# Kernel tuning notes

Measured on AMD Instinct MI355X. Metric: run time of the kernel, lower is better.

The kernel has to match this reference:

```python
import jax, jax.numpy as jnp
import numpy as np

N, E, D, H, DH, FF, C, L = 50000, 640000, 128, 8, 16, 256, 5, 6
EPS = 1e-5


def _bn(x, g, b):
    # training-mode BatchNorm1d over the node dimension
    m = jnp.mean(x, axis=0)
    v = jnp.var(x, axis=0)
    return (x - m) * jax.lax.rsqrt(v + EPS) * g + b


def _sparse_mha(x, src, dst, Wq, Wk, Wv, Wo):
    # edge-restricted multi-head attention: softmax over incoming edges per dst node
    q = (x @ Wq).reshape(N, H, DH)
    k = (x @ Wk).reshape(N, H, DH)
    v = (x @ Wv).reshape(N, H, DH)
    s = jnp.einsum('ehd,ehd->eh', q[dst], k[src]) * (1.0 / np.sqrt(DH))  # [E,H]
    smax = jax.ops.segment_max(s, dst, num_segments=N)
    smax = jnp.where(jnp.isfinite(smax), smax, 0.0)  # guard isolated nodes
    e = jnp.exp(s - smax[dst])
    den = jax.ops.segment_sum(e, dst, num_segments=N)
    alpha = e / jnp.where(den > 0, den, 1.0)[dst]
    out = jax.ops.segment_sum(alpha[:, :, None] * v[src], dst, num_segments=N)  # [N,H,DH]
    return out.reshape(N, D) @ Wo


def setup_inputs() -> dict:
    key = jax.random.key(0)
    ks = jax.random.split(key, 18)
    f = lambda k, shp, sc: (jax.random.normal(k, shp, jnp.float32) * sc)
    return {
        'x': jax.random.normal(ks[0], (N, D), jnp.float32),
        'edge_index': jax.random.randint(ks[1], (2, E), 0, N),
        'Wq': f(ks[2], (L, D, D), 0.08),
        'Wk': f(ks[3], (L, D, D), 0.08),
        'Wv': f(ks[4], (L, D, D), 0.08),
        'Wo': f(ks[5], (L, D, D), 0.08),
        'g1': jnp.ones((L, D), jnp.float32),
        'bn1': jnp.zeros((L, D), jnp.float32),
        'W1': f(ks[6], (L, D, FF), 0.08),
        'bf1': jnp.zeros((L, FF), jnp.float32),
        'W2': f(ks[7], (L, FF, D), 0.06),
        'bf2': jnp.zeros((L, D), jnp.float32),
        'g2': jnp.ones((L, D), jnp.float32),
        'bn2': jnp.zeros((L, D), jnp.float32),
        'Wp': f(ks[8], (D, C), 0.08),
        'bp': jnp.zeros((C,), jnp.float32),
    }


def reference(x, edge_index, Wq, Wk, Wv, Wo, g1, bn1, W1, bf1, W2, bf2, g2, bn2, Wp, bp):
    src, dst = edge_index[0], edge_index[1]
    for i in range(L):  # fixed small layer count
        res = x  # residual is Identity (num_input == num_output)
        a = _sparse_mha(x, src, dst, Wq[i], Wk[i], Wv[i], Wo[i])
        x = _bn(a + res, g1[i], bn1[i])
        h = jax.nn.relu(x @ W1[i] + bf1[i])  # leakiness=0 -> relu
        x = _bn(x + (h @ W2[i] + bf2[i]), g2[i], bn2[i])
    node_pred = x @ Wp + bp
    return node_pred
```

## Files before the change

kernel.cpp:

```cpp
#include <hip/hip_runtime.h>
#include <hip/hip_bf16.h>
#include <cstdio>

#define NN 50000
#define EE 640000
#define DD 128
#define HH 8
#define DH 16
#define FFD 256
#define CC 5
#define LL 6
#define EPSV 1e-5f

typedef __attribute__((ext_vector_type(8))) short bf16x8;
typedef __attribute__((ext_vector_type(8))) unsigned short ushort8;
typedef __attribute__((ext_vector_type(4))) float f32x4;

__device__ __forceinline__ float bfu2f(unsigned short u) {
  union { unsigned int i; float f; } x; x.i = ((unsigned int)u) << 16; return x.f;
}
__device__ __forceinline__ unsigned short f2bf(float f) {
  union { float f; unsigned int i; } x; x.f = f;
  unsigned int r = (x.i + 0x7fffu + ((x.i >> 16) & 1u)) >> 16;
  return (unsigned short)r;
}

__global__ void detect_kernel(const unsigned int* __restrict__ g1w, int* __restrict__ flag) {
  if (threadIdx.x == 0 && blockIdx.x == 0) *flag = (g1w[0] == 0x3F803F80u) ? 1 : 0;
}

struct ConvJobs { const void* in[8]; float* out[8]; int n[8]; };
__global__ __launch_bounds__(256) void convert_batch_kernel(ConvJobs jobs, const int* __restrict__ flag) {
  int b = blockIdx.x;
  const void* in = jobs.in[b];
  float* out = jobs.out[b];
  int n = jobs.n[b];
  int use_bf = *flag;
  for (int i = threadIdx.x; i < n; i += 256) {
    if (use_bf) out[i] = bfu2f(((const unsigned short*)in)[i]);
    else        out[i] = ((const float*)in)[i];
  }
}

__global__ __launch_bounds__(256) void to_bf16_kernel(const void* __restrict__ in,
                                                      unsigned short* __restrict__ out, int n,
                                                      const int* __restrict__ flag) {
  int i = blockIdx.x * blockDim.x + threadIdx.x;
  if (i >= n) return;
  if (*flag) out[i] = ((const unsigned short*)in)[i];
  else       out[i] = f2bf(((const float*)in)[i]);
}

__global__ __launch_bounds__(256) void t_qkv_tiled(const void* __restrict__ wq, const void* __restrict__ wk,
                                                   const void* __restrict__ wv,
                                                   unsigned short* __restrict__ qkvT,
                                                   const int* __restrict__ flag) {
  __shared__ unsigned short tile[32][33];
  int l = blockIdx.z / 3, which = blockIdx.z % 3;
  const void* in = (which == 0) ? wq : (which == 1) ? wk : wv;
  size_t off = (size_t)l * DD * DD;
  unsigned short* out = qkvT + (size_t)l * 384 * DD + (size_t)which * DD * DD;
  int tx = threadIdx.x & 31, ty = threadIdx.x >> 5;
  int k0 = blockIdx.x * 32, n0 = blockIdx.y * 32;
  int use_bf = *flag;
#pragma unroll
  for (int i = 0; i < 4; i++) {
    int k = k0 + ty + i * 8;
    unsigned short v;
    if (use_bf) v = ((const unsigned short*)in)[off + (size_t)k * DD + n0 + tx];
    else        v = f2bf(((const float*)in)[off + (size_t)k * DD + n0 + tx]);
    tile[ty + i * 8][tx] = v;
  }
  __syncthreads();
#pragma unroll
  for (int i = 0; i < 4; i++) {
    int n = n0 + ty + i * 8;
    out[(size_t)n * DD + k0 + tx] = tile[tx][ty + i * 8];
  }
}

__global__ __launch_bounds__(256) void t_w_tiled(const void* __restrict__ in,
                                                 unsigned short* __restrict__ out,
                                                 int K, int N, const int* __restrict__ flag) {
  __shared__ unsigned short tile[32][33];
  int l = blockIdx.z;
  size_t off = (size_t)l * K * N;
  unsigned short* o = out + (size_t)l * K * N;
  int tx = threadIdx.x & 31, ty = threadIdx.x >> 5;
  int k0 = blockIdx.x * 32, n0 = blockIdx.y * 32;
  int use_bf = *flag;
#pragma unroll
  for (int i = 0; i < 4; i++) {
    int k = k0 + ty + i * 8;
    unsigned short v;
    if (use_bf) v = ((const unsigned short*)in)[off + (size_t)k * N + n0 + tx];
    else        v = f2bf(((const float*)in)[off + (size_t)k * N + n0 + tx]);
    tile[ty + i * 8][tx] = v;
  }
  __syncthreads();
#pragma unroll
  for (int i = 0; i < 4; i++) {
    int n = n0 + ty + i * 8;
    o[(size_t)n * K + k0 + tx] = tile[tx][ty + i * 8];
  }
}

__global__ __launch_bounds__(256) void zero_kernel(int* __restrict__ p, int n) {
  int i = blockIdx.x * blockDim.x + threadIdx.x;
  if (i < n) p[i] = 0;
}

__global__ void init_id_kernel(float* __restrict__ stats_id, float* __restrict__ g_id, float* __restrict__ b_id) {
  int t = threadIdx.x;
  if (t < 128) {
    stats_id[t] = 0.f;
    stats_id[128 + t] = (float)NN * (1.0f - EPSV);
    g_id[t] = 1.f;
    b_id[t] = 0.f;
  }
}

__global__ __launch_bounds__(256) void count_kernel(const int* __restrict__ dst, int* __restrict__ counts) {
  int e = blockIdx.x * blockDim.x + threadIdx.x;
  if (e < EE) atomicAdd(&counts[dst[e]], 1);
}

__global__ __launch_bounds__(256) void scan1_kernel(const int* __restrict__ counts,
                                                    int* __restrict__ row_ptr, int* __restrict__ partials) {
  __shared__ int sh[256];
  int t = threadIdx.x;
  int i = blockIdx.x * 256 + t;
  int v = (i < NN) ? counts[i] : 0;
  sh[t] = v; __syncthreads();
#pragma unroll
  for (int off = 1; off < 256; off <<= 1) {
    int u = (t >= off) ? sh[t - off] : 0;
    __syncthreads();
    sh[t] += u;
    __syncthreads();
  }
  if (i < NN) row_ptr[i] = sh[t] - v;
  if (t == 255) partials[blockIdx.x] = sh[t];
}

__global__ __launch_bounds__(256) void scan2_kernel(int* __restrict__ partials, int nb) {
  __shared__ int sh[256];
  int t = threadIdx.x;
  int v = (t < nb) ? partials[t] : 0;
  sh[t] = v; __syncthreads();
#pragma unroll
  for (int off = 1; off < 256; off <<= 1) {
    int u = (t >= off) ? sh[t - off] : 0;
    __syncthreads();
    sh[t] += u;
    __syncthreads();
  }
  if (t < nb) partials[t] = sh[t] - v;
}

__global__ __launch_bounds__(256) void scan3_kernel(int* __restrict__ row_ptr, const int* __restrict__ partials) {
  int i = blockIdx.x * 256 + threadIdx.x;
  if (i < NN) row_ptr[i] += partials[blockIdx.x];
  if (i == 0) row_ptr[NN] = EE;
}

__global__ __launch_bounds__(256) void fill_kernel(const int* __restrict__ src, const int* __restrict__ dst,
                                                   const int* __restrict__ row_ptr, int* __restrict__ cursor,
                                                   int* __restrict__ csr_src) {
  int e = blockIdx.x * blockDim.x + threadIdx.x;
  if (e < EE) {
    int d = dst[e];
    int pos = row_ptr[d] + atomicAdd(&cursor[d], 1);
    csr_src[pos] = src[e];
  }
}

__global__ __launch_bounds__(128) void fold_kernel(const float* __restrict__ stats,
                                                   const float* __restrict__ g,
                                                   const float* __restrict__ b,
                                                   const unsigned short* __restrict__ WT,
                                                   const float* __restrict__ base_bias,
                                                   unsigned short* __restrict__ WTo,
                                                   float* __restrict__ bias_o,
                                                   float* __restrict__ ss_o) {
  __shared__ float ssc[128];
  __shared__ float ssh[128];
  __shared__ float part[2];
  int t = threadIdx.x;
  float mean = stats[t] * (1.f / NN);
  float var  = fmaxf(stats[128 + t] * (1.f / NN) - mean * mean, 0.f);
  float sc = g[t] * rsqrtf(var + EPSV);
  float sh = b[t] - mean * sc;
  ssc[t] = sc; ssh[t] = sh;
  if (blockIdx.x == 0) { ss_o[t] = sc; ss_o[128 + t] = sh; }
  __syncthreads();
  int c = blockIdx.x;
  float w = bfu2f(WT[(size_t)c * 128 + t]);
  WTo[(size_t)c * 128 + t] = f2bf(ssc[t] * w);
  float contrib = ssh[t] * w;
#pragma unroll
  for (int off = 32; off; off >>= 1) contrib += __shfl_down(contrib, off);
  if ((t & 63) == 0) part[t >> 6] = contrib;
  __syncthreads();
  if (t == 0) bias_o[c] = (base_bias ? base_bias[c] : 0.f) + part[0] + part[1];
}

template<int NTILES, bool RELU>
__global__ __launch_bounds__(256) void mfma_gemm_nt(const unsigned short* __restrict__ A,
                                                    const unsigned short* __restrict__ BT,
                                                    const float* __restrict__ bias,
                                                    unsigned short* __restrict__ C,
                                                    int M, int ldc) {
  const int K = 128;
  int tid = threadIdx.x;
  int lane = tid & 63, wave = tid >> 6;
  int m0 = blockIdx.x * 128 + wave * 32;
  int nbase = blockIdx.y * (NTILES * 64);
  int lm = lane & 15;
  int quad = lane >> 4;
  int kq = quad * 8;

  int rowA[2];
#pragma unroll
  for (int r = 0; r < 2; r++) {
    int rr = m0 + 16 * r + lm;
    rowA[r] = (rr < M) ? rr : (M - 1);
  }
  bf16x8 a[2][4];
#pragma unroll
  for (int ks = 0; ks < 4; ks++) {
    a[0][ks] = *(const bf16x8*)(A + (size_t)rowA[0] * K + ks * 32 + kq);
    a[1][ks] = *(const bf16x8*)(A + (size_t)rowA[1] * K + ks * 32 + kq);
  }

#pragma unroll
  for (int nt = 0; nt < NTILES; nt++) {
    int n0 = nbase + nt * 64;
    bf16x8 b[4][4];
#pragma unroll
    for (int c = 0; c < 4; c++)
#pragma unroll
      for (int ks = 0; ks < 4; ks++)
        b[c][ks] = *(const bf16x8*)(BT + (size_t)(n0 + 16 * c + lm) * K + ks * 32 + kq);

    f32x4 acc[2][4];
#pragma unroll
    for (int r = 0; r < 2; r++)
#pragma unroll
      for (int c = 0; c < 4; c++) acc[r][c] = (f32x4){0.f, 0.f, 0.f, 0.f};
#pragma unroll
    for (int ks = 0; ks < 4; ks++)
#pragma unroll
      for (int r = 0; r < 2; r++)
#pragma unroll
        for (int c = 0; c < 4; c++)
          acc[r][c] = __builtin_amdgcn_mfma_f32_16x16x32_bf16(b[c][ks], a[r][ks], acc[r][c], 0, 0, 0);

#pragma unroll
    for (int r = 0; r < 2; r++) {
      int row = m0 + 16 * r + lm;
      if (row >= M) continue;
#pragma unroll
      for (int c = 0; c < 4; c++) {
        int col = n0 + 16 * c + quad * 4;
        float4 bv = *(const float4*)(bias + col);
        float o[4];
        o[0] = acc[r][c][0] + bv.x; o[1] = acc[r][c][1] + bv.y;
        o[2] = acc[r][c][2] + bv.z; o[3] = acc[r][c][3] + bv.w;
        if (RELU) {
          o[0] = fmaxf(o[0], 0.f); o[1] = fmaxf(o[1], 0.f);
          o[2] = fmaxf(o[2], 0.f); o[3] = fmaxf(o[3], 0.f);
        }
        ushort4 w;
        w.x = f2bf(o[0]); w.y = f2bf(o[1]); w.z = f2bf(o[2]); w.w = f2bf(o[3]);
        *(ushort4*)(C + (size_t)row * ldc + col) = w;
      }
    }
  }
}

template<int K, bool RELU, bool HASBIAS, bool RESAFF, bool STATS>
__global__ __launch_bounds__(256) void mfma_gemm(const unsigned short* __restrict__ A,
                                                 const unsigned short* __restrict__ BT,
                                                 const float* __restrict__ bias,
                                                 const unsigned short* __restrict__ resid,
                                                 const float* __restrict__ rss,
                                                 unsigned short* __restrict__ C,
                                                 float* __restrict__ stats,
                                                 int M, int ldc) {
  __shared__ float lsum[64];
  __shared__ float lsq[64];
  int tid = threadIdx.x;
  int lane = tid & 63, wave = tid >> 6;
  int m0 = blockIdx.x * 128 + wave * 32;
  int n0 = blockIdx.y * 64;
  int lm = lane & 15;
  int quad = lane >> 4;
  int kq = quad * 8;

  int rowA[2];
#pragma unroll
  for (int r = 0; r < 2; r++) {
    int rr = m0 + 16 * r + lm;
    rowA[r] = (rr < M) ? rr : (M - 1);
  }
  const unsigned short* aptr0 = A + (size_t)rowA[0] * K + kq;
  const unsigned short* aptr1 = A + (size_t)rowA[1] * K + kq;
  const unsigned short* bptr[4];
#pragma unroll
  for (int c = 0; c < 4; c++)
    bptr[c] = BT + (size_t)(n0 + 16 * c + lm) * K + kq;

  f32x4 acc[2][4];
#pragma unroll
  for (int r = 0; r < 2; r++)
#pragma unroll
    for (int c = 0; c < 4; c++) acc[r][c] = (f32x4){0.f, 0.f, 0.f, 0.f};

#pragma unroll
  for (int kc = 0; kc < K; kc += 128) {
    bf16x8 a[2][4], b[4][4];
#pragma unroll
    for (int ks = 0; ks < 4; ks++) {
      a[0][ks] = *(const bf16x8*)(aptr0 + kc + ks * 32);
      a[1][ks] = *(const bf16x8*)(aptr1 + kc + ks * 32);
    }
#pragma unroll
    for (int c = 0; c < 4; c++)
#pragma unroll
      for (int ks = 0; ks < 4; ks++)
        b[c][ks] = *(const bf16x8*)(bptr[c] + kc + ks * 32);
#pragma unroll
    for (int ks = 0; ks < 4; ks++)
#pragma unroll
      for (int r = 0; r < 2; r++)
#pragma unroll
        for (int c = 0; c < 4; c++)
          acc[r][c] = __builtin_amdgcn_mfma_f32_16x16x32_bf16(b[c][ks], a[r][ks], acc[r][c], 0, 0, 0);
  }

  if (STATS) {
    if (tid < 64) { lsum[tid] = 0.f; lsq[tid] = 0.f; }
    __syncthreads();
  }

  float st_s[4][4], st_q[4][4];
  if (STATS) {
#pragma unroll
    for (int c = 0; c < 4; c++)
#pragma unroll
      for (int reg = 0; reg < 4; reg++) { st_s[c][reg] = 0.f; st_q[c][reg] = 0.f; }
  }

#pragma unroll
  for (int r = 0; r < 2; r++) {
    int row = m0 + 16 * r + lm;
    if (row >= M) continue;
#pragma unroll
    for (int c = 0; c < 4; c++) {
      int col = n0 + 16 * c + quad * 4;
      float4 bv = HASBIAS ? *(const float4*)(bias + col) : make_float4(0.f, 0.f, 0.f, 0.f);
      float o[4];
      o[0] = acc[r][c][0] + bv.x; o[1] = acc[r][c][1] + bv.y;
      o[2] = acc[r][c][2] + bv.z; o[3] = acc[r][c][3] + bv.w;
      if (RESAFF) {
        ushort4 rr = *(const ushort4*)(resid + (size_t)row * ldc + col);
        float4 rsc = *(const float4*)(rss + col);
        float4 rsh = *(const float4*)(rss + 128 + col);
        o[0] += bfu2f(rr.x) * rsc.x + rsh.x;
        o[1] += bfu2f(rr.y) * rsc.y + rsh.y;
        o[2] += bfu2f(rr.z) * rsc.z + rsh.z;
        o[3] += bfu2f(rr.w) * rsc.w + rsh.w;
      }
      if (RELU) {
        o[0] = fmaxf(o[0], 0.f); o[1] = fmaxf(o[1], 0.f);
        o[2] = fmaxf(o[2], 0.f); o[3] = fmaxf(o[3], 0.f);
      }
      size_t idx = (size_t)row * ldc + col;
      ushort4 w;
      w.x = f2bf(o[0]); w.y = f2bf(o[1]); w.z = f2bf(o[2]); w.w = f2bf(o[3]);
      *(ushort4*)(C + idx) = w;
      if (STATS) {
#pragma unroll
        for (int reg = 0; reg < 4; reg++) {
          st_s[c][reg] += o[reg];
          st_q[c][reg] = fmaf(o[reg], o[reg], st_q[c][reg]);
        }
      }
    }
  }

  if (STATS) {
#pragma unroll
    for (int c = 0; c < 4; c++)
#pragma unroll
      for (int reg = 0; reg < 4; reg++) {
        float s = st_s[c][reg], q = st_q[c][reg];
        s += __shfl_xor(s, 1);  q += __shfl_xor(q, 1);
        s += __shfl_xor(s, 2);  q += __shfl_xor(q, 2);
        s += __shfl_xor(s, 4);  q += __shfl_xor(q, 4);
        s += __shfl_xor(s, 8);  q += __shfl_xor(q, 8);
        if (lm == 0) {
          atomicAdd(&lsum[16 * c + quad * 4 + reg], s);
          atomicAdd(&lsq[16 * c + quad * 4 + reg], q);
        }
      }
    __syncthreads();
    if (tid < 64) {
      atomicAdd(&stats[n0 + tid], lsum[tid]);
      atomicAdd(&stats[128 + n0 + tid], lsq[tid]);
    }
  }
}

__global__ __launch_bounds__(256) void attn_kernel(const unsigned short* __restrict__ qkv,
                                                   const int* __restrict__ row_ptr,
                                                   const int* __restrict__ csr_src,
                                                   unsigned short* __restrict__ t1) {
  int t = blockIdx.x * blockDim.x + threadIdx.x;
  int half = t & 1;
  int nh = t >> 1;
  int n = nh >> 3, h = nh & 7;
  const unsigned short* qp = qkv + (size_t)n * 384 + h * 16 + half * 8;
  float qf[8];
  {
    bf16x8 q0 = *(const bf16x8*)qp;
#pragma unroll
    for (int i = 0; i < 8; i++) qf[i] = bfu2f((unsigned short)q0[i]);
  }
  float m = -3.0e38f, l = 0.f;
  float A[8];
#pragma unroll
  for (int i = 0; i < 8; i++) A[i] = 0.f;
  int e0 = row_ptr[n], e1 = row_ptr[n + 1];
  if (e0 < e1) {
    int last = e1 - 1;
    const size_t hoff = 128 + h * 16 + half * 8;
    int s0 = csr_src[e0];
    const unsigned short* kp0 = qkv + (size_t)s0 * 384 + hoff;
    bf16x8 ck = *(const bf16x8*)kp0;
    bf16x8 cv = *(const bf16x8*)(kp0 + 128);
    int ei1 = (e0 + 1 <= last) ? e0 + 1 : last;
    int s1 = csr_src[ei1];
    const unsigned short* kp1 = qkv + (size_t)s1 * 384 + hoff;
    bf16x8 nk = *(const bf16x8*)kp1;
    bf16x8 nv = *(const bf16x8*)(kp1 + 128);
    for (int e = e0; e < e1; e++) {
      int e2 = (e + 2 <= last) ? e + 2 : last;
      int s2 = csr_src[e2];
      const unsigned short* kp2 = qkv + (size_t)s2 * 384 + hoff;
      bf16x8 k2 = *(const bf16x8*)kp2;
      bf16x8 v2 = *(const bf16x8*)(kp2 + 128);

      float part = 0.f;
#pragma unroll
      for (int i = 0; i < 8; i++) part += qf[i] * bfu2f((unsigned short)ck[i]);
      float sc = (part + __shfl_xor(part, 1)) * 0.25f;
      float mn = fmaxf(m, sc);
      float cf = __expf(m - mn);
      float p  = __expf(sc - mn);
      l = l * cf + p;
#pragma unroll
      for (int i = 0; i < 8; i++)
        A[i] = A[i] * cf + p * bfu2f((unsigned short)cv[i]);
      m = mn;
      ck = nk; cv = nv; nk = k2; nv = v2;
    }
  }
  float inv = (l > 0.f) ? 1.f / l : 0.f;
  ushort8 o0;
#pragma unroll
  for (int i = 0; i < 8; i++) o0[i] = f2bf(A[i] * inv);
  unsigned short* op = t1 + (size_t)n * 128 + h * 16 + half * 8;
  *(ushort8*)op = o0;
}

__global__ __launch_bounds__(256) void proj_kernel(const unsigned short* __restrict__ y2,
                                                   const float* __restrict__ statsL,
                                                   const float* __restrict__ g,
                                                   const float* __restrict__ b,
                                                   const float* __restrict__ Wp,
                                                   const float* __restrict__ bp,
                                                   void* __restrict__ out,
                                                   const int* __restrict__ flag) {
  __shared__ float W[DD * CC];
  __shared__ float bias[CC];
  __shared__ float ssc[128];
  __shared__ float ssh[128];
  int t = threadIdx.x;
  for (int i = t; i < DD * CC; i += 256) W[i] = Wp[i];
  if (t < CC) bias[t] = bp[t];
  if (t < 128) {
    float mean = statsL[t] * (1.f / NN);
    float var  = fmaxf(statsL[128 + t] * (1.f / NN) - mean * mean, 0.f);
    float sc = g[t] * rsqrtf(var + EPSV);
    ssc[t] = sc;
    ssh[t] = b[t] - mean * sc;
  }
  __syncthreads();
  int n = blockIdx.x * 256 + t;
  if (n >= NN) return;
  float acc[CC];
#pragma unroll
  for (int c = 0; c < CC; c++) acc[c] = bias[c];
  const ushort4* xp = (const ushort4*)(y2 + (size_t)n * DD);
#pragma unroll
  for (int k4 = 0; k4 < DD / 4; k4++) {
    ushort4 u = xp[k4];
    int k = k4 * 4;
    float a0 = bfu2f(u.x) * ssc[k + 0] + ssh[k + 0];
    float a1 = bfu2f(u.y) * ssc[k + 1] + ssh[k + 1];
    float a2 = bfu2f(u.z) * ssc[k + 2] + ssh[k + 2];
    float a3 = bfu2f(u.w) * ssc[k + 3] + ssh[k + 3];
    const float* w = &W[k * CC];
#pragma unroll
    for (int c = 0; c < CC; c++)
      acc[c] += a0 * w[c] + a1 * w[CC + c] + a2 * w[2 * CC + c] + a3 * w[3 * CC + c];
  }
  if (*flag) {
    __hip_bfloat16* o16 = (__hip_bfloat16*)out;
#pragma unroll
    for (int c = 0; c < CC; c++) o16[(size_t)n * CC + c] = __float2bfloat16(acc[c]);
  } else {
    float* o32 = (float*)out;
#pragma unroll
    for (int c = 0; c < CC; c++) o32[(size_t)n * CC + c] = acc[c];
  }
}

extern "C" void kernel_launch(void* const* d_in, const int* in_sizes, int n_in,
                              void* d_out, int out_size, void* d_ws, size_t ws_size,
                              hipStream_t stream) {
  const int* ei = (const int*)d_in[1];

  char* p = (char*)d_ws;
  auto carve = [&](size_t bytes) { char* r = p; p += (bytes + 255) & ~(size_t)255; return (void*)r; };
  unsigned short* xb   = (unsigned short*)carve((size_t)NN * DD * 2);
  unsigned short* qkv  = (unsigned short*)carve((size_t)NN * 384 * 2);
  unsigned short* t1   = (unsigned short*)carve((size_t)NN * DD * 2);
  unsigned short* hbuf = (unsigned short*)carve((size_t)NN * FFD * 2);
  unsigned short* y1   = (unsigned short*)carve((size_t)NN * DD * 2);
  unsigned short* y2   = (unsigned short*)carve((size_t)NN * DD * 2);
  float* stats  = (float*)carve(12 * 256 * 4);
  float* stats_id = (float*)carve(256 * 4);
  float* ss     = (float*)carve(12 * 256 * 4);
  float* ss_id  = (float*)carve(256 * 4);
  float* g_id   = (float*)carve(128 * 4);
  float* b_id   = (float*)carve(128 * 4);
  int* row_ptr = (int*)carve((size_t)(NN + 1) * 4);
  int* cursor  = (int*)carve((size_t)NN * 4);
  int* counts  = (int*)carve((size_t)NN * 4);
  int* csr_src = (int*)carve((size_t)EE * 4);
  int* flag    = (int*)carve(256);
  int* partials = (int*)carve(256 * 4);
  unsigned short* qkvT = (unsigned short*)carve((size_t)LL * 384 * DD * 2);
  unsigned short* WoT  = (unsigned short*)carve((size_t)LL * DD * DD * 2);
  unsigned short* W1T  = (unsigned short*)carve((size_t)LL * FFD * DD * 2);
  unsigned short* W2T  = (unsigned short*)carve((size_t)LL * DD * FFD * 2);
  unsigned short* qkvTf = (unsigned short*)carve((size_t)384 * DD * 2);
  unsigned short* W1Tf  = (unsigned short*)carve((size_t)FFD * DD * 2);
  float* qkv_bias = (float*)carve(384 * 4);
  float* w1_bias  = (float*)carve(256 * 4);
  float* g1_f  = (float*)carve((size_t)LL * DD * 4);
  float* bn1_f = (float*)carve((size_t)LL * DD * 4);
  float* bf1_f = (float*)carve((size_t)LL * FFD * 4);
  float* bf2_f = (float*)carve((size_t)LL * DD * 4);
  float* g2_f  = (float*)carve((size_t)LL * DD * 4);
  float* bn2_f = (float*)carve((size_t)LL * DD * 4);
  float* Wp_f  = (float*)carve((size_t)DD * CC * 4);
  float* bp_f  = (float*)carve((size_t)CC * 4);
  size_t need = (size_t)(p - (char*)d_ws);
  if (need > ws_size) {
    fprintf(stderr, "kernel_launch: workspace too small: need %zu, have %zu\n", need, ws_size);
    return;
  }

  const int* src  = ei;
  const int* dstp = ei + EE;

  detect_kernel<<<1, 64, 0, stream>>>((const unsigned int*)d_in[6], flag);
  to_bf16_kernel<<<(NN * DD + 255) / 256, 256, 0, stream>>>(d_in[0], xb, NN * DD, flag);

  {
    ConvJobs j;
    j.in[0] = d_in[6];  j.out[0] = g1_f;  j.n[0] = LL * DD;
    j.in[1] = d_in[7];  j.out[1] = bn1_f; j.n[1] = LL * DD;
    j.in[2] = d_in[9];  j.out[2] = bf1_f; j.n[2] = LL * FFD;
    j.in[3] = d_in[11]; j.out[3] = bf2_f; j.n[3] = LL * DD;
    j.in[4] = d_in[12]; j.out[4] = g2_f;  j.n[4] = LL * DD;
    j.in[5] = d_in[13]; j.out[5] = bn2_f; j.n[5] = LL * DD;
    j.in[6] = d_in[14]; j.out[6] = Wp_f;  j.n[6] = DD * CC;
    j.in[7] = d_in[15]; j.out[7] = bp_f;  j.n[7] = CC;
    convert_batch_kernel<<<8, 256, 0, stream>>>(j, flag);
  }

  t_qkv_tiled<<<dim3(4, 4, 3 * LL), 256, 0, stream>>>(d_in[2], d_in[3], d_in[4], qkvT, flag);
  t_w_tiled<<<dim3(4, 4, LL), 256, 0, stream>>>(d_in[5], WoT, DD, DD, flag);
  t_w_tiled<<<dim3(4, 8, LL), 256, 0, stream>>>(d_in[8], W1T, DD, FFD, flag);
  t_w_tiled<<<dim3(8, 4, LL), 256, 0, stream>>>(d_in[10], W2T, FFD, DD, flag);

  zero_kernel<<<12, 256, 0, stream>>>((int*)stats, 12 * 256);
  init_id_kernel<<<1, 128, 0, stream>>>(stats_id, g_id, b_id);
  zero_kernel<<<(NN + 255) / 256, 256, 0, stream>>>(counts, NN);
  zero_kernel<<<(NN + 255) / 256, 256, 0, stream>>>(cursor, NN);

  const int NB = (NN + 255) / 256;
  count_kernel<<<(EE + 255) / 256, 256, 0, stream>>>(dstp, counts);
  scan1_kernel<<<NB, 256, 0, stream>>>(counts, row_ptr, partials);
  scan2_kernel<<<1, 256, 0, stream>>>(partials, NB);
  scan3_kernel<<<NB, 256, 0, stream>>>(row_ptr, partials);
  fill_kernel<<<(EE + 255) / 256, 256, 0, stream>>>(src, dstp, row_ptr, cursor, csr_src);

  const int gm = (NN + 127) / 128;
  for (int layer = 0; layer < LL; layer++) {
    const unsigned short* WoT_l = WoT + (size_t)layer * DD * DD;
    const unsigned short* W1T_l = W1T + (size_t)layer * FFD * DD;
    const unsigned short* W2T_l = W2T + (size_t)layer * DD * FFD;
    float* st1 = stats + (size_t)(layer * 2 + 0) * 256;
    float* st2 = stats + (size_t)(layer * 2 + 1) * 256;
    float* ss1 = ss + (size_t)(layer * 2 + 0) * 256;

    const unsigned short* Ain = layer ? y2 : xb;
    const float* stats_prev = layer ? (stats + (size_t)((layer - 1) * 2 + 1) * 256) : stats_id;
    const float* g_prev = layer ? (g2_f + (size_t)(layer - 1) * DD) : g_id;
    const float* b_prev = layer ? (bn2_f + (size_t)(layer - 1) * DD) : b_id;
    float* ss_prev = layer ? (ss + (size_t)((layer - 1) * 2 + 1) * 256) : ss_id;

    fold_kernel<<<384, 128, 0, stream>>>(stats_prev, g_prev, b_prev,
                                         qkvT + (size_t)layer * 384 * DD, nullptr,
                                         qkvTf, qkv_bias, ss_prev);
    mfma_gemm_nt<3, false><<<dim3(gm, 2), 256, 0, stream>>>(
        Ain, qkvTf, qkv_bias, qkv, NN, 384);
    attn_kernel<<<NN * HH * 2 / 256, 256, 0, stream>>>(qkv, row_ptr, csr_src, t1);
    mfma_gemm<128, false, false, true, true><<<dim3(gm, 2), 256, 0, stream>>>(
        t1, WoT_l, nullptr, Ain, ss_prev, y1, st1, NN, 128);
    fold_kernel<<<256, 128, 0, stream>>>(st1, g1_f + (size_t)layer * DD, bn1_f + (size_t)layer * DD,
                                         W1T_l, bf1_f + (size_t)layer * FFD,
                                         W1Tf, w1_bias, ss1);
    mfma_gemm_nt<2, true><<<dim3(gm, 2), 256, 0, stream>>>(
        y1, W1Tf, w1_bias, hbuf, NN, 256);
    mfma_gemm<256, false, true, true, true><<<dim3(gm, 2), 256, 0, stream>>>(
        hbuf, W2T_l, bf2_f + (size_t)layer * DD, y1, ss1, y2, st2, NN, 128);
  }

  proj_kernel<<<(NN + 255) / 256, 256, 0, stream>>>(
      y2, stats + (size_t)((LL - 1) * 2 + 1) * 256, g2_f + (size_t)(LL - 1) * DD,
      bn2_f + (size_t)(LL - 1) * DD, Wp_f, bp_f, d_out, flag);
}
```

Measured before the change: 1.389 ms.

## Fuse FFN GEMMs through LDS and route QKV projection through generic GEMM

Adds an ffn_fused kernel that computes relu(y1·W1+b1) into a padded LDS tile and immediately multiplies it by W2, adding the BN-affine residual and accumulating batch-norm statistics. The intermediate hidden activation no longer round-trips through global memory, and one launch per layer goes away. The QKV projection now uses the generic mfma_gemm with a 6-wide column grid instead of the removed NT kernel. The cost is about 67KB of LDS per block and a larger per-block workload, which reduces occupancy.

```diff
diff --git a/kernel.cpp b/kernel.cpp
--- a/kernel.cpp
+++ b/kernel.cpp
@@ -11,6 +11,7 @@
 #define CC 5
 #define LL 6
 #define EPSV 1e-5f
+#define HPAD 264
 
 typedef __attribute__((ext_vector_type(8))) short bf16x8;
 typedef __attribute__((ext_vector_type(8))) unsigned short ushort8;
@@ -203,80 +204,6 @@
   if ((t & 63) == 0) part[t >> 6] = contrib;
   __syncthreads();
   if (t == 0) bias_o[c] = (base_bias ? base_bias[c] : 0.f) + part[0] + part[1];
-}
-
-template<int NTILES, bool RELU>
-__global__ __launch_bounds__(256) void mfma_gemm_nt(const unsigned short* __restrict__ A,
-                                                    const unsigned short* __restrict__ BT,
-                                                    const float* __restrict__ bias,
-                                                    unsigned short* __restrict__ C,
-                                                    int M, int ldc) {
-  const int K = 128;
-  int tid = threadIdx.x;
-  int lane = tid & 63, wave = tid >> 6;
-  int m0 = blockIdx.x * 128 + wave * 32;
-  int nbase = blockIdx.y * (NTILES * 64);
-  int lm = lane & 15;
-  int quad = lane >> 4;
-  int kq = quad * 8;
-
-  int rowA[2];
-#pragma unroll
-  for (int r = 0; r < 2; r++) {
-    int rr = m0 + 16 * r + lm;
-    rowA[r] = (rr < M) ? rr : (M - 1);
-  }
-  bf16x8 a[2][4];
-#pragma unroll
-  for (int ks = 0; ks < 4; ks++) {
-    a[0][ks] = *(const bf16x8*)(A + (size_t)rowA[0] * K + ks * 32 + kq);
-    a[1][ks] = *(const bf16x8*)(A + (size_t)rowA[1] * K + ks * 32 + kq);
-  }
-
-#pragma unroll
-  for (int nt = 0; nt < NTILES; nt++) {
-    int n0 = nbase + nt * 64;
-    bf16x8 b[4][4];
-#pragma unroll
-    for (int c = 0; c < 4; c++)
-#pragma unroll
-      for (int ks = 0; ks < 4; ks++)
-        b[c][ks] = *(const bf16x8*)(BT + (size_t)(n0 + 16 * c + lm) * K + ks * 32 + kq);
-
-    f32x4 acc[2][4];
-#pragma unroll
-    for (int r = 0; r < 2; r++)
-#pragma unroll
-      for (int c = 0; c < 4; c++) acc[r][c] = (f32x4){0.f, 0.f, 0.f, 0.f};
-#pragma unroll
-    for (int ks = 0; ks < 4; ks++)
-#pragma unroll
-      for (int r = 0; r < 2; r++)
-#pragma unroll
-        for (int c = 0; c < 4; c++)
-          acc[r][c] = __builtin_amdgcn_mfma_f32_16x16x32_bf16(b[c][ks], a[r][ks], acc[r][c], 0, 0, 0);
-
-#pragma unroll
-    for (int r = 0; r < 2; r++) {
-      int row = m0 + 16 * r + lm;
-      if (row >= M) continue;
-#pragma unroll
-      for (int c = 0; c < 4; c++) {
-        int col = n0 + 16 * c + quad * 4;
-        float4 bv = *(const float4*)(bias + col);
-        float o[4];
-        o[0] = acc[r][c][0] + bv.x; o[1] = acc[r][c][1] + bv.y;
-        o[2] = acc[r][c][2] + bv.z; o[3] = acc[r][c][3] + bv.w;
-        if (RELU) {
-          o[0] = fmaxf(o[0], 0.f); o[1] = fmaxf(o[1], 0.f);
-          o[2] = fmaxf(o[2], 0.f); o[3] = fmaxf(o[3], 0.f);
-        }
-        ushort4 w;
-        w.x = f2bf(o[0]); w.y = f2bf(o[1]); w.z = f2bf(o[2]); w.w = f2bf(o[3]);
-        *(ushort4*)(C + (size_t)row * ldc + col) = w;
-      }
-    }
-  }
 }
 
 template<int K, bool RELU, bool HASBIAS, bool RESAFF, bool STATS>
@@ -413,6 +340,162 @@
   }
 }
 
+__global__ __launch_bounds__(256) void ffn_fused(const unsigned short* __restrict__ A,
+                                                 const unsigned short* __restrict__ W1T,
+                                                 const float* __restrict__ b1,
+                                                 const unsigned short* __restrict__ W2T,
+                                                 const float* __restrict__ b2,
+                                                 const float* __restrict__ rss,
+                                                 unsigned short* __restrict__ C,
+                                                 float* __restrict__ stats, int M) {
+  __shared__ unsigned short hl[128 * HPAD];
+  __shared__ float lsum[128];
+  __shared__ float lsq[128];
+  int tid = threadIdx.x;
+  int lane = tid & 63, wave = tid >> 6;
+  int m0 = blockIdx.x * 128 + wave * 32;
+  int lm = lane & 15, quad = lane >> 4, kq = quad * 8;
+
+  if (tid < 128) { lsum[tid] = 0.f; lsq[tid] = 0.f; }
+  __syncthreads();
+
+  int rowA[2];
+#pragma unroll
+  for (int r = 0; r < 2; r++) {
+    int rr = m0 + 16 * r + lm;
+    rowA[r] = (rr < M) ? rr : (M - 1);
+  }
+  bf16x8 a[2][4];
+#pragma unroll
+  for (int ks = 0; ks < 4; ks++) {
+    a[0][ks] = *(const bf16x8*)(A + (size_t)rowA[0] * 128 + ks * 32 + kq);
+    a[1][ks] = *(const bf16x8*)(A + (size_t)rowA[1] * 128 + ks * 32 + kq);
+  }
+
+#pragma unroll
+  for (int nt = 0; nt < 4; nt++) {
+    int n0 = nt * 64;
+    bf16x8 b[4][4];
+#pragma unroll
+    for (int c = 0; c < 4; c++)
+#pragma unroll
+      for (int ks = 0; ks < 4; ks++)
+        b[c][ks] = *(const bf16x8*)(W1T + (size_t)(n0 + 16 * c + lm) * 128 + ks * 32 + kq);
+    f32x4 acc[2][4];
+#pragma unroll
+    for (int r = 0; r < 2; r++)
+#pragma unroll
+      for (int c = 0; c < 4; c++) acc[r][c] = (f32x4){0.f, 0.f, 0.f, 0.f};
+#pragma unroll
+    for (int ks = 0; ks < 4; ks++)
+#pragma unroll
+      for (int r = 0; r < 2; r++)
+#pragma unroll
+        for (int c = 0; c < 4; c++)
+          acc[r][c] = __builtin_amdgcn_mfma_f32_16x16x32_bf16(b[c][ks], a[r][ks], acc[r][c], 0, 0, 0);
+#pragma unroll
+    for (int r = 0; r < 2; r++) {
+      int lrow = wave * 32 + 16 * r + lm;
+#pragma unroll
+      for (int c = 0; c < 4; c++) {
+        int col = n0 + 16 * c + quad * 4;
+        float4 bv = *(const float4*)(b1 + col);
+        ushort4 w;
+        w.x = f2bf(fmaxf(acc[r][c][0] + bv.x, 0.f));
+        w.y = f2bf(fmaxf(acc[r][c][1] + bv.y, 0.f));
+        w.z = f2bf(fmaxf(acc[r][c][2] + bv.z, 0.f));
+        w.w = f2bf(fmaxf(acc[r][c][3] + bv.w, 0.f));
+        *(ushort4*)(hl + (size_t)lrow * HPAD + col) = w;
+      }
+    }
+  }
+
+#pragma unroll
+  for (int nt = 0; nt < 2; nt++) {
+    int n0 = nt * 64;
+    f32x4 acc[2][4];
+#pragma unroll
+    for (int r = 0; r < 2; r++)
+#pragma unroll
+      for (int c = 0; c < 4; c++) acc[r][c] = (f32x4){0.f, 0.f, 0.f, 0.f};
+#pragma unroll
+    for (int kc = 0; kc < 256; kc += 128) {
+      bf16x8 ha[2][4], b[4][4];
+#pragma unroll
+      for (int ks = 0; ks < 4; ks++) {
+        ha[0][ks] = *(const bf16x8*)(hl + (size_t)(wave * 32 + lm) * HPAD + kc + ks * 32 + kq);
+        ha[1][ks] = *(const bf16x8*)(hl + (size_t)(wave * 32 + 16 + lm) * HPAD + kc + ks * 32 + kq);
+      }
+#pragma unroll
+      for (int c = 0; c < 4; c++)
+#pragma unroll
+        for (int ks = 0; ks < 4; ks++)
+          b[c][ks] = *(const bf16x8*)(W2T + (size_t)(n0 + 16 * c + lm) * 256 + kc + ks * 32 + kq);
+#pragma unroll
+      for (int ks = 0; ks < 4; ks++)
+#pragma unroll
+        for (int r = 0; r < 2; r++)
+#pragma unroll
+          for (int c = 0; c < 4; c++)
+            acc[r][c] = __builtin_amdgcn_mfma_f32_16x16x32_bf16(b[c][ks], ha[r][ks], acc[r][c], 0, 0, 0);
+    }
+
+    float st_s[4][4], st_q[4][4];
+#pragma unroll
+    for (int c = 0; c < 4; c++)
+#pragma unroll
+      for (int reg = 0; reg < 4; reg++) { st_s[c][reg] = 0.f; st_q[c][reg] = 0.f; }
+
+#pragma unroll
+    for (int r = 0; r < 2; r++) {
+      int row = m0 + 16 * r + lm;
+      if (row >= M) continue;
+#pragma unroll
+      for (int c = 0; c < 4; c++) {
+        int col = n0 + 16 * c + quad * 4;
+        float4 bv = *(const float4*)(b2 + col);
+        float o[4];
+        o[0] = acc[r][c][0] + bv.x; o[1] = acc[r][c][1] + bv.y;
+        o[2] = acc[r][c][2] + bv.z; o[3] = acc[r][c][3] + bv.w;
+        ushort4 rr = *(const ushort4*)(A + (size_t)row * 128 + col);
+        float4 rsc = *(const float4*)(rss + col);
+        float4 rsh = *(const float4*)(rss + 128 + col);
+        o[0] += bfu2f(rr.x) * rsc.x + rsh.x;
+        o[1] += bfu2f(rr.y) * rsc.y + rsh.y;
+        o[2] += bfu2f(rr.z) * rsc.z + rsh.z;
+        o[3] += bfu2f(rr.w) * rsc.w + rsh.w;
+        ushort4 w;
+        w.x = f2bf(o[0]); w.y = f2bf(o[1]); w.z = f2bf(o[2]); w.w = f2bf(o[3]);
+        *(ushort4*)(C + (size_t)row * 128 + col) = w;
+#pragma unroll
+        for (int reg = 0; reg < 4; reg++) {
+          st_s[c][reg] += o[reg];
+          st_q[c][reg] = fmaf(o[reg], o[reg], st_q[c][reg]);
+        }
+      }
+    }
+#pragma unroll
+    for (int c = 0; c < 4; c++)
+#pragma unroll
+      for (int reg = 0; reg < 4; reg++) {
+        float s = st_s[c][reg], q = st_q[c][reg];
+        s += __shfl_xor(s, 1);  q += __shfl_xor(q, 1);
+        s += __shfl_xor(s, 2);  q += __shfl_xor(q, 2);
+        s += __shfl_xor(s, 4);  q += __shfl_xor(q, 4);
+        s += __shfl_xor(s, 8);  q += __shfl_xor(q, 8);
+        if (lm == 0) {
+          atomicAdd(&lsum[n0 + 16 * c + quad * 4 + reg], s);
+          atomicAdd(&lsq[n0 + 16 * c + quad * 4 + reg], q);
+        }
+      }
+  }
+  __syncthreads();
+  if (tid < 128) {
+    atomicAdd(&stats[tid], lsum[tid]);
+    atomicAdd(&stats[128 + tid], lsq[tid]);
+  }
+}
+
 __global__ __launch_bounds__(256) void attn_kernel(const unsigned short* __restrict__ qkv,
                                                    const int* __restrict__ row_ptr,
                                                    const int* __restrict__ csr_src,
@@ -435,7 +518,7 @@
   int e0 = row_ptr[n], e1 = row_ptr[n + 1];
   if (e0 < e1) {
     int last = e1 - 1;
-    const size_t hoff = 128 + h * 16 + half * 8;
+    const size_t hoff = 128 + (size_t)h * 16 + half * 8;
     int s0 = csr_src[e0];
     const unsigned short* kp0 = qkv + (size_t)s0 * 384 + hoff;
     bf16x8 ck = *(const bf16x8*)kp0;
@@ -538,7 +621,6 @@
   unsigned short* xb   = (unsigned short*)carve((size_t)NN * DD * 2);
   unsigned short* qkv  = (unsigned short*)carve((size_t)NN * 384 * 2);
   unsigned short* t1   = (unsigned short*)carve((size_t)NN * DD * 2);
-  unsigned short* hbuf = (unsigned short*)carve((size_t)NN * FFD * 2);
   unsigned short* y1   = (unsigned short*)carve((size_t)NN * DD * 2);
   unsigned short* y2   = (unsigned short*)carve((size_t)NN * DD * 2);
   float* stats  = (float*)carve(12 * 256 * 4);
@@ -629,18 +711,16 @@
     fold_kernel<<<384, 128, 0, stream>>>(stats_prev, g_prev, b_prev,
                                          qkvT + (size_t)layer * 384 * DD, nullptr,
                                          qkvTf, qkv_bias, ss_prev);
-    mfma_gemm_nt<3, false><<<dim3(gm, 2), 256, 0, stream>>>(
-        Ain, qkvTf, qkv_bias, qkv, NN, 384);
+    mfma_gemm<128, false, true, false, false><<<dim3(gm, 6), 256, 0, stream>>>(
+        Ain, qkvTf, qkv_bias, nullptr, nullptr, qkv, nullptr, NN, 384);
     attn_kernel<<<NN * HH * 2 / 256, 256, 0, stream>>>(qkv, row_ptr, csr_src, t1);
     mfma_gemm<128, false, false, true, true><<<dim3(gm, 2), 256, 0, stream>>>(
         t1, WoT_l, nullptr, Ain, ss_prev, y1, st1, NN, 128);
     fold_kernel<<<256, 128, 0, stream>>>(st1, g1_f + (size_t)layer * DD, bn1_f + (size_t)layer * DD,
                                          W1T_l, bf1_f + (size_t)layer * FFD,
                                          W1Tf, w1_bias, ss1);
-    mfma_gemm_nt<2, true><<<dim3(gm, 2), 256, 0, stream>>>(
-        y1, W1Tf, w1_bias, hbuf, NN, 256);
-    mfma_gemm<256, false, true, true, true><<<dim3(gm, 2), 256, 0, stream>>>(
-        hbuf, W2T_l, bf2_f + (size_t)layer * DD, y1, ss1, y2, st2, NN, 128);
+    ffn_fused<<<gm, 256, 0, stream>>>(y1, W1Tf, w1_bias, W2T_l,
+                                      bf2_f + (size_t)layer * DD, ss1, y2, st2, NN);
   }
 
   proj_kernel<<<(NN + 255) / 256, 256, 0, stream>>>(
```

Result: faster. 1.248 ms (-10.1%).
